# Kernel optimization log

Measured on AMD Instinct MI355X. Metric: run time of the kernel, lower is better.

## Reference

```python
import jax, jax.numpy as jnp
import numpy as np

N, E = 50000, 800000
NODE_DIM, EDGE_DIM, HIDDEN = 128, 32, 128


def setup_inputs() -> dict:
    key = jax.random.key(0)
    ks = jax.random.split(key, 12)
    def lin(k, fan_in, shape):
        bound = 1.0 / np.sqrt(fan_in)
        return jax.random.uniform(k, shape, jnp.float32, -bound, bound)
    return {
        "x": jax.random.normal(ks[0], (N, NODE_DIM), jnp.float32),
        "edge_index": jax.random.randint(ks[1], (2, E), 0, N),
        "edge_attr": jax.random.normal(ks[2], (E, EDGE_DIM), jnp.float32),
        # msg MLP: Linear(node+edge -> hidden), Linear(hidden -> hidden)
        "W1": lin(ks[3], NODE_DIM + EDGE_DIM, (HIDDEN, NODE_DIM + EDGE_DIM)),
        "b1": lin(ks[4], NODE_DIM + EDGE_DIM, (HIDDEN,)),
        "W2": lin(ks[5], HIDDEN, (HIDDEN, HIDDEN)),
        "b2": lin(ks[6], HIDDEN, (HIDDEN,)),
        # GRUCell(input=HIDDEN, hidden=NODE_DIM); gate order r,z,n (torch)
        "W_ih": lin(ks[7], NODE_DIM, (3 * NODE_DIM, HIDDEN)),
        "b_ih": lin(ks[8], NODE_DIM, (3 * NODE_DIM,)),
        "W_hh": lin(ks[9], NODE_DIM, (3 * NODE_DIM, NODE_DIM)),
        "b_hh": lin(ks[10], NODE_DIM, (3 * NODE_DIM,)),
    }


def reference(x, edge_index, edge_attr, W1, b1, W2, b2, W_ih, b_ih, W_hh, b_hh):
    src, dst = edge_index[0], edge_index[1]
    # gather + edge MLP: [E, node+edge] -> [E, hidden]
    m_in = jnp.concatenate([x[src], edge_attr], axis=-1)
    h1 = jax.nn.silu(m_in @ W1.T + b1)
    m = jax.nn.silu(h1 @ W2.T + b2)
    # scatter-add messages per destination node
    agg = jax.ops.segment_sum(m, dst, num_segments=x.shape[0])  # [N, hidden]
    # GRUCell: gates in torch order (r, z, n)
    gi = agg @ W_ih.T + b_ih  # [N, 3*node_dim]
    gh = x @ W_hh.T + b_hh
    i_r, i_z, i_n = jnp.split(gi, 3, axis=-1)
    h_r, h_z, h_n = jnp.split(gh, 3, axis=-1)
    r = jax.nn.sigmoid(i_r + h_r)
    z = jax.nn.sigmoid(i_z + h_z)
    n = jnp.tanh(i_n + r * h_n)
    return (1.0 - z) * n + z * x
```

## Files before the change

### kernel.cpp

```cpp
#include <hip/hip_runtime.h>
#include <hip/hip_bf16.h>
#include <cstdint>

typedef __bf16 bf16x8 __attribute__((ext_vector_type(8)));
typedef __bf16 bf16x4 __attribute__((ext_vector_type(4)));
typedef float  f32x4  __attribute__((ext_vector_type(4)));

#define ND 128
#define HID 128

__device__ __forceinline__ f32x4 mfma_bf16(bf16x8 a, bf16x8 b, f32x4 c) {
  return __builtin_amdgcn_mfma_f32_16x16x32_bf16(a, b, c, 0, 0, 0);
}
__device__ __forceinline__ float fast_sigmoid(float x) {
  return __fdividef(1.f, 1.f + __expf(-x));
}
__device__ __forceinline__ float fast_silu(float x) {
  return __fdividef(x, 1.f + __expf(-x));
}
__device__ __forceinline__ float fast_tanh(float x) {
  float cx = fminf(fmaxf(x, -15.f), 15.f);
  float e = __expf(2.f * cx);
  return __fdividef(e - 1.f, e + 1.f);
}

__global__ void cvt_all(const float* __restrict__ s0, __bf16* __restrict__ d0, int c1,
                        const float* __restrict__ s1, __bf16* __restrict__ d1, int c2,
                        const float* __restrict__ s2, __bf16* __restrict__ d2, int c3,
                        const float* __restrict__ s3, __bf16* __restrict__ d3, int c4,
                        const float* __restrict__ s4, __bf16* __restrict__ d4, int c5) {
  int i = blockIdx.x * blockDim.x + threadIdx.x;
  const float* s; __bf16* d; int j;
  if (i < c1)      { s = s0; d = d0; j = i; }
  else if (i < c2) { s = s1; d = d1; j = i - c1; }
  else if (i < c3) { s = s2; d = d2; j = i - c2; }
  else if (i < c4) { s = s3; d = d3; j = i - c3; }
  else if (i < c5) { s = s4; d = d4; j = i - c4; }
  else return;
  const float4* sp = reinterpret_cast<const float4*>(s) + (size_t)j * 2;
  float4 a = sp[0], b = sp[1];
  bf16x8 v;
  v[0] = (__bf16)a.x; v[1] = (__bf16)a.y; v[2] = (__bf16)a.z; v[3] = (__bf16)a.w;
  v[4] = (__bf16)b.x; v[5] = (__bf16)b.y; v[6] = (__bf16)b.z; v[7] = (__bf16)b.w;
  reinterpret_cast<bf16x8*>(d)[j] = v;
}

__global__ void k_hist(const int* __restrict__ dst, int* __restrict__ counts, int E) {
  int e = blockIdx.x * 256 + threadIdx.x;
  if (e < E) atomicAdd(&counts[dst[e]], 1);
}

__global__ void k_blocksum(const int* __restrict__ counts, int* __restrict__ bsum) {
  __shared__ int sd[256];
  int t = threadIdx.x;
  sd[t] = counts[blockIdx.x * 256 + t];
  __syncthreads();
  for (int d = 128; d > 0; d >>= 1) { if (t < d) sd[t] += sd[t + d]; __syncthreads(); }
  if (!t) bsum[blockIdx.x] = sd[0];
}

__global__ void k_scan_bsum(int* __restrict__ bsum, int nb) {
  __shared__ int sd[256];
  int t = threadIdx.x;
  int v = (t < nb) ? bsum[t] : 0;
  sd[t] = v;
  __syncthreads();
  for (int d = 1; d < 256; d <<= 1) {
    int u = (t >= d) ? sd[t - d] : 0;
    __syncthreads();
    sd[t] += u;
    __syncthreads();
  }
  if (t < nb) bsum[t] = sd[t] - v;
}

__global__ void k_scan_write(const int* __restrict__ counts, const int* __restrict__ bsum,
                             int* __restrict__ cursor) {
  __shared__ int sd[256];
  int t = threadIdx.x, b = blockIdx.x;
  int i = b * 256 + t;
  int c = counts[i];
  sd[t] = c;
  __syncthreads();
  for (int d = 1; d < 256; d <<= 1) {
    int u = (t >= d) ? sd[t - d] : 0;
    __syncthreads();
    sd[t] += u;
    __syncthreads();
  }
  cursor[i] = bsum[b] + sd[t] - c;
}

__global__ void k_perm(const int* __restrict__ dst, int* __restrict__ cursor,
                       int* __restrict__ eperm, int* __restrict__ dsorted, int E) {
  int e = blockIdx.x * 256 + threadIdx.x;
  if (e < E) {
    int d = dst[e];
    int p = atomicAdd(&cursor[d], 1);
    eperm[p] = e;
    dsorted[p] = d;
  }
}

#define TILE_E 64

__global__ __launch_bounds__(512, 4) void edge_mlp2(
    const __bf16* __restrict__ xb,
    const int*    __restrict__ srcp,
    const float*  __restrict__ ea,
    const __bf16* __restrict__ W1b,
    const float*  __restrict__ b1,
    const __bf16* __restrict__ W2b,
    const float*  __restrict__ b2,
    const int*    __restrict__ eperm,
    const int*    __restrict__ dsorted,
    float* __restrict__ agg,
    int ntiles)
{
  __shared__ __bf16 Als[TILE_E * 160];
  __shared__ __bf16 H1[TILE_E * 128];
  __shared__ int dstls[TILE_E];
  char* AB = (char*)Als;
  char* HB = (char*)H1;

  const int tid = threadIdx.x;
  const int w  = tid >> 6;
  const int l  = tid & 63;
  const int l4 = l >> 4;
  const int lm = l & 15;
  const int jb = w * 16;

  bf16x8 bw1[5], bw2[4];
  {
    const int jr = jb + lm;
#pragma unroll
    for (int kt = 0; kt < 5; ++kt)
      bw1[kt] = *reinterpret_cast<const bf16x8*>(W1b + (size_t)jr * 160 + kt * 32 + l4 * 8);
#pragma unroll
    for (int kt = 0; kt < 4; ++kt)
      bw2[kt] = *reinterpret_cast<const bf16x8*>(W2b + (size_t)jr * 128 + kt * 32 + l4 * 8);
  }
  const float4 b1v = *reinterpret_cast<const float4*>(b1 + jb + l4 * 4);
  const float4 b2v = *reinterpret_cast<const float4*>(b2 + jb + l4 * 4);

  const int fj = tid & 127;
  const int fg = tid >> 7;
  const int fchunk = fj >> 3;
  const int finner = (fj & 7) * 2;

  const int xslot = tid >> 4, xq = tid & 15;
  const int aslot = tid >> 3, aq = tid & 7;

  bf16x8 pxv0 = {}, pxv1 = {};
  float4 pea_ = {};
  int pdst_ = 0;

  auto PREFETCH = [&](int t) {
    int p0 = t * TILE_E;
    int e0i = eperm[p0 + xslot];
    int e1i = eperm[p0 + xslot + 32];
    int s0 = srcp[e0i];
    int s1 = srcp[e1i];
    pxv0 = *reinterpret_cast<const bf16x8*>(xb + (size_t)s0 * ND + xq * 8);
    pxv1 = *reinterpret_cast<const bf16x8*>(xb + (size_t)s1 * ND + xq * 8);
    int e2i = eperm[p0 + aslot];
    pea_ = reinterpret_cast<const float4*>(ea)[(size_t)e2i * 8 + aq];
    if (tid < TILE_E) pdst_ = dsorted[p0 + tid];
  };

  int tile = blockIdx.x;
  if (tile < ntiles) PREFETCH(tile);

  for (; tile < ntiles; tile += gridDim.x) {
    __syncthreads();

    {
      int s_ = xslot;
      *reinterpret_cast<bf16x8*>(AB + s_ * 320 + ((xq ^ (s_ & 7)) << 4)) = pxv0;
      int s2 = xslot + 32;
      *reinterpret_cast<bf16x8*>(AB + s2 * 320 + ((xq ^ (s2 & 7)) << 4)) = pxv1;
    }
    {
      bf16x4 h;
      h[0] = (__bf16)pea_.x; h[1] = (__bf16)pea_.y;
      h[2] = (__bf16)pea_.z; h[3] = (__bf16)pea_.w;
      int pc = 16 + ((aq >> 1) ^ (aslot & 3));
      *reinterpret_cast<bf16x4*>(AB + aslot * 320 + (pc << 4) + ((aq & 1) << 3)) = h;
    }
    if (tid < TILE_E) dstls[tid] = pdst_;
    __syncthreads();

    int nt = tile + gridDim.x;
    if (nt < ntiles) PREFETCH(nt);

#pragma unroll
    for (int et = 0; et < 4; ++et) {
      const int s_ = et * 16 + lm;
      const int sw = s_ & 7;
      f32x4 acc = {0.f, 0.f, 0.f, 0.f};
#pragma unroll
      for (int kt = 0; kt < 4; ++kt) {
        bf16x8 bfrag = *reinterpret_cast<const bf16x8*>(AB + s_ * 320 + (((kt * 4 + l4) ^ sw) << 4));
        acc = mfma_bf16(bw1[kt], bfrag, acc);
      }
      {
        bf16x8 bfrag = *reinterpret_cast<const bf16x8*>(AB + s_ * 320 + ((16 + (l4 ^ (s_ & 3))) << 4));
        acc = mfma_bf16(bw1[4], bfrag, acc);
      }
      bf16x4 h0;
#pragma unroll
      for (int rr = 0; rr < 4; ++rr)
        h0[rr] = (__bf16)fast_silu(acc[rr] + (&b1v.x)[rr]);
      int c0 = w * 2 + (l4 >> 1);
      int inner = (l4 & 1) << 3;
      *reinterpret_cast<bf16x4*>(HB + s_ * 256 + ((c0 ^ sw) << 4) + inner) = h0;
    }
    __syncthreads();

#pragma unroll
    for (int et = 0; et < 4; ++et) {
      const int s_ = et * 16 + lm;
      const int sw = s_ & 7;
      f32x4 acc = {0.f, 0.f, 0.f, 0.f};
#pragma unroll
      for (int kt = 0; kt < 4; ++kt) {
        bf16x8 bfrag = *reinterpret_cast<const bf16x8*>(HB + s_ * 256 + (((kt * 4 + l4) ^ sw) << 4));
        acc = mfma_bf16(bw2[kt], bfrag, acc);
      }
      bf16x4 m0;
#pragma unroll
      for (int rr = 0; rr < 4; ++rr)
        m0[rr] = (__bf16)fast_silu(acc[rr] + (&b2v.x)[rr]);
      int c0 = w * 2 + (l4 >> 1);
      int inner = (l4 & 1) << 3;
      *reinterpret_cast<bf16x4*>(AB + s_ * 256 + ((c0 ^ sw) << 4) + inner) = m0;
    }
    __syncthreads();

    {
      float acc = 0.f;
      int cur = dstls[fg * 16];
#pragma unroll
      for (int i = 0; i < 16; ++i) {
        int slot = fg * 16 + i;
        int nd = dstls[slot];
        if (nd != cur) {
          atomicAdd(agg + (size_t)cur * HID + fj, acc);
          acc = 0.f;
          cur = nd;
        }
        uint32_t raw = *reinterpret_cast<const uint16_t*>(
            AB + slot * 256 + ((fchunk ^ (slot & 7)) << 4) + finner);
        acc += __uint_as_float(raw << 16);
      }
      atomicAdd(agg + (size_t)cur * HID + fj, acc);
    }
  }
}

__global__ __launch_bounds__(512) void gru2(
    const float*  __restrict__ agg,
    const __bf16* __restrict__ xb,
    const float*  __restrict__ x,
    const __bf16* __restrict__ Wih, const float* __restrict__ bih,
    const __bf16* __restrict__ Whh, const float* __restrict__ bhh,
    float* __restrict__ out, int N)
{
  const int tid = threadIdx.x;
  const int w = tid >> 6, l = tid & 63;
  const int l4 = l >> 4, lm = l & 15;
  const int n0 = blockIdx.x * 64;
  const int jb = w * 16;
  const int jr = jb + lm, jz = jr + 128, jn = jr + 256;

  bf16x8 WiR[4], WhR[4], WiZ[4], WhZ[4], WiN[4], WhN[4];
#pragma unroll
  for (int kt = 0; kt < 4; ++kt) {
    int ko = kt * 32 + l4 * 8;
    WiR[kt] = *reinterpret_cast<const bf16x8*>(Wih + (size_t)jr * ND + ko);
    WhR[kt] = *reinterpret_cast<const bf16x8*>(Whh + (size_t)jr * ND + ko);
    WiZ[kt] = *reinterpret_cast<const bf16x8*>(Wih + (size_t)jz * ND + ko);
    WhZ[kt] = *reinterpret_cast<const bf16x8*>(Whh + (size_t)jz * ND + ko);
    WiN[kt] = *reinterpret_cast<const bf16x8*>(Wih + (size_t)jn * ND + ko);
    WhN[kt] = *reinterpret_cast<const bf16x8*>(Whh + (size_t)jn * ND + ko);
  }
  float4 birv, bizv, binv, bhnv;
  {
    int j0 = jb + l4 * 4;
    float4 a = *reinterpret_cast<const float4*>(bih + j0);
    float4 b = *reinterpret_cast<const float4*>(bhh + j0);
    birv = make_float4(a.x + b.x, a.y + b.y, a.z + b.z, a.w + b.w);
    a = *reinterpret_cast<const float4*>(bih + 128 + j0);
    b = *reinterpret_cast<const float4*>(bhh + 128 + j0);
    bizv = make_float4(a.x + b.x, a.y + b.y, a.z + b.z, a.w + b.w);
    binv = *reinterpret_cast<const float4*>(bih + 256 + j0);
    bhnv = *reinterpret_cast<const float4*>(bhh + 256 + j0);
  }

#pragma unroll
  for (int rt = 0; rt < 4; ++rt) {
    const int node = n0 + rt * 16 + lm;
    const bool ok = node < N;
    bf16x8 aA[4], aX[4];
#pragma unroll
    for (int kt = 0; kt < 4; ++kt) {
      int ko = kt * 32 + l4 * 8;
      bf16x8 z8 = {};
      if (ok) {
        float4 a0 = *reinterpret_cast<const float4*>(agg + (size_t)node * ND + ko);
        float4 a1 = *reinterpret_cast<const float4*>(agg + (size_t)node * ND + ko + 4);
        bf16x8 v;
        v[0] = (__bf16)a0.x; v[1] = (__bf16)a0.y; v[2] = (__bf16)a0.z; v[3] = (__bf16)a0.w;
        v[4] = (__bf16)a1.x; v[5] = (__bf16)a1.y; v[6] = (__bf16)a1.z; v[7] = (__bf16)a1.w;
        aA[kt] = v;
        aX[kt] = *reinterpret_cast<const bf16x8*>(xb + (size_t)node * ND + ko);
      } else {
        aA[kt] = z8;
        aX[kt] = z8;
      }
    }
    f32x4 aR = {0.f,0.f,0.f,0.f}, aZ = {0.f,0.f,0.f,0.f};
    f32x4 ai = {0.f,0.f,0.f,0.f}, ah = {0.f,0.f,0.f,0.f};
#pragma unroll
    for (int kt = 0; kt < 4; ++kt) {
      aR = mfma_bf16(WiR[kt], aA[kt], aR);
      aR = mfma_bf16(WhR[kt], aX[kt], aR);
      aZ = mfma_bf16(WiZ[kt], aA[kt], aZ);
      aZ = mfma_bf16(WhZ[kt], aX[kt], aZ);
      ai = mfma_bf16(WiN[kt], aA[kt], ai);
      ah = mfma_bf16(WhN[kt], aX[kt], ah);
    }
    if (ok) {
      float4 xv = *reinterpret_cast<const float4*>(x + (size_t)node * ND + jb + l4 * 4);
      float4 ov;
#pragma unroll
      for (int rr = 0; rr < 4; ++rr) {
        float r = fast_sigmoid(aR[rr] + (&birv.x)[rr]);
        float z = fast_sigmoid(aZ[rr] + (&bizv.x)[rr]);
        float n = fast_tanh(ai[rr] + (&binv.x)[rr] + r * (ah[rr] + (&bhnv.x)[rr]));
        (&ov.x)[rr] = (1.f - z) * n + z * (&xv.x)[rr];
      }
      *reinterpret_cast<float4*>(out + (size_t)node * ND + jb + l4 * 4) = ov;
    }
  }
}

extern "C" void kernel_launch(void* const* d_in, const int* in_sizes, int n_in,
                              void* d_out, int out_size, void* d_ws, size_t ws_size,
                              hipStream_t stream) {
  const float* x   = (const float*)d_in[0];
  const int*   ei  = (const int*)d_in[1];
  const float* ea  = (const float*)d_in[2];
  const float* W1  = (const float*)d_in[3];
  const float* b1  = (const float*)d_in[4];
  const float* W2  = (const float*)d_in[5];
  const float* b2  = (const float*)d_in[6];
  const float* Wih = (const float*)d_in[7];
  const float* bih = (const float*)d_in[8];
  const float* Whh = (const float*)d_in[9];
  const float* bhh = (const float*)d_in[10];
  float* out = (float*)d_out;
  const int N = in_sizes[0] / ND;
  const int E = in_sizes[1] / 2;

  const int nb = (N + 255) / 256;
  const int nC = nb * 256;

  char* ws = (char*)d_ws;
  size_t off = 0;
  auto alloc = [&](size_t bytes) -> void* {
    void* p = ws + off;
    off += (bytes + 255) & ~(size_t)255;
    return p;
  };
  __bf16* xb      = (__bf16*)alloc((size_t)N * ND * 2);
  __bf16* W1b     = (__bf16*)alloc(128 * 160 * 2);
  __bf16* W2b     = (__bf16*)alloc(128 * 128 * 2);
  __bf16* Wihb    = (__bf16*)alloc(384 * 128 * 2);
  __bf16* Whhb    = (__bf16*)alloc(384 * 128 * 2);
  int*    counts  = (int*)alloc((size_t)nC * 4);
  int*    cursor  = (int*)alloc((size_t)nC * 4);
  int*    bsum    = (int*)alloc(256 * 4);
  int*    eperm   = (int*)alloc((size_t)E * 4);
  int*    dsorted = (int*)alloc((size_t)E * 4);
  float*  agg     = (float*)alloc((size_t)N * ND * 4);
  (void)ws_size;

  const int* srcp = ei;
  const int* dstp = ei + E;

  hipMemsetAsync(agg, 0, (size_t)N * ND * 4, stream);
  hipMemsetAsync(counts, 0, (size_t)nC * 4, stream);

  const int n8_x = N * ND / 8, n8_1 = 128 * 160 / 8, n8_2 = 128 * 128 / 8, n8_g = 384 * 128 / 8;
  int c1 = n8_x, c2 = c1 + n8_1, c3 = c2 + n8_2, c4 = c3 + n8_g, c5 = c4 + n8_g;
  cvt_all<<<(c5 + 255) / 256, 256, 0, stream>>>(x, xb, c1, W1, W1b, c2, W2, W2b, c3,
                                                Wih, Wihb, c4, Whh, Whhb, c5);

  k_hist<<<(E + 255) / 256, 256, 0, stream>>>(dstp, counts, E);
  k_blocksum<<<nb, 256, 0, stream>>>(counts, bsum);
  k_scan_bsum<<<1, 256, 0, stream>>>(bsum, nb);
  k_scan_write<<<nb, 256, 0, stream>>>(counts, bsum, cursor);
  k_perm<<<(E + 255) / 256, 256, 0, stream>>>(dstp, cursor, eperm, dsorted, E);

  const int ntiles = E / TILE_E;
  edge_mlp2<<<2500, 512, 0, stream>>>(xb, srcp, ea, W1b, b1, W2b, b2,
                                      eperm, dsorted, agg, ntiles);

  gru2<<<(N + 63) / 64, 512, 0, stream>>>(agg, xb, x, Wihb, bih, Whhb, bhh, out, N);
}
```

Before: 365.8 us.

## Switch edge MLP to 32x32x16 MFMA tiles and restructure scatter reduction

The edge MLP kernel now uses 32x32x16 bf16 MFMA, with each wave computing a 32-hidden by 32-edge tile instead of four 16x16 tiles. Bias is preloaded into the accumulator, and the LDS swizzle widens to 16 chunks. The segmented scatter-add now runs on only four waves, each lane holding two columns and reading dst via readlane. Edge-attribute loads are deferred, so only the index is prefetched. Together these aim to cut MFMA issue count and LDS reads per edge, at the cost of more weight registers, which may hurt occupancy. Bias is also rounded to bf16, which slightly lowers precision.

```diff
diff --git a/kernel.cpp b/kernel.cpp
--- a/kernel.cpp
+++ b/kernel.cpp
@@ -5,12 +5,14 @@
 typedef __bf16 bf16x8 __attribute__((ext_vector_type(8)));
 typedef __bf16 bf16x4 __attribute__((ext_vector_type(4)));
 typedef float  f32x4  __attribute__((ext_vector_type(4)));
+typedef float  f32x16 __attribute__((ext_vector_type(16)));
+typedef unsigned short u16x16 __attribute__((ext_vector_type(16)));
 
 #define ND 128
 #define HID 128
 
-__device__ __forceinline__ f32x4 mfma_bf16(bf16x8 a, bf16x8 b, f32x4 c) {
-  return __builtin_amdgcn_mfma_f32_16x16x32_bf16(a, b, c, 0, 0, 0);
+__device__ __forceinline__ f32x16 mfma32(bf16x8 a, bf16x8 b, f32x16 c) {
+  return __builtin_amdgcn_mfma_f32_32x32x16_bf16(a, b, c, 0, 0, 0);
 }
 __device__ __forceinline__ float fast_sigmoid(float x) {
   return __fdividef(1.f, 1.f + __expf(-x));
@@ -22,6 +24,9 @@
   float cx = fminf(fmaxf(x, -15.f), 15.f);
   float e = __expf(2.f * cx);
   return __fdividef(e - 1.f, e + 1.f);
+}
+__device__ __forceinline__ f32x4 mfma_bf16(bf16x8 a, bf16x8 b, f32x4 c) {
+  return __builtin_amdgcn_mfma_f32_16x16x32_bf16(a, b, c, 0, 0, 0);
 }
 
 __global__ void cvt_all(const float* __restrict__ s0, __bf16* __restrict__ d0, int c1,
@@ -104,7 +109,7 @@
 
 #define TILE_E 64
 
-__global__ __launch_bounds__(512, 4) void edge_mlp2(
+__global__ __launch_bounds__(512, 4) void edge_mlp3(
     const __bf16* __restrict__ xb,
     const int*    __restrict__ srcp,
     const float*  __restrict__ ea,
@@ -124,47 +129,49 @@
   char* HB = (char*)H1;
 
   const int tid = threadIdx.x;
-  const int w  = tid >> 6;
-  const int l  = tid & 63;
-  const int l4 = l >> 4;
-  const int lm = l & 15;
-  const int jb = w * 16;
-
-  bf16x8 bw1[5], bw2[4];
+  const int w   = tid >> 6;
+  const int l   = tid & 63;
+  const int hi  = l >> 5;
+  const int sl  = l & 31;
+  const int jb  = (w & 3) * 32;
+  const int sh  = (w >> 2) * 32;
+  const int s   = sh + sl;
+  const int sw  = s & 15;
+
+  bf16x8 bw1[10], bw2[8];
   {
-    const int jr = jb + lm;
-#pragma unroll
-    for (int kt = 0; kt < 5; ++kt)
-      bw1[kt] = *reinterpret_cast<const bf16x8*>(W1b + (size_t)jr * 160 + kt * 32 + l4 * 8);
-#pragma unroll
-    for (int kt = 0; kt < 4; ++kt)
-      bw2[kt] = *reinterpret_cast<const bf16x8*>(W2b + (size_t)jr * 128 + kt * 32 + l4 * 8);
-  }
-  const float4 b1v = *reinterpret_cast<const float4*>(b1 + jb + l4 * 4);
-  const float4 b2v = *reinterpret_cast<const float4*>(b2 + jb + l4 * 4);
-
-  const int fj = tid & 127;
-  const int fg = tid >> 7;
-  const int fchunk = fj >> 3;
-  const int finner = (fj & 7) * 2;
+    const int jr = jb + sl;
+#pragma unroll
+    for (int kt = 0; kt < 10; ++kt)
+      bw1[kt] = *reinterpret_cast<const bf16x8*>(W1b + (size_t)jr * 160 + kt * 16 + hi * 8);
+#pragma unroll
+    for (int kt = 0; kt < 8; ++kt)
+      bw2[kt] = *reinterpret_cast<const bf16x8*>(W2b + (size_t)jr * 128 + kt * 16 + hi * 8);
+  }
+  u16x16 b1p, b2p;
+#pragma unroll
+  for (int g = 0; g < 4; ++g) {
+#pragma unroll
+    for (int r = 0; r < 4; ++r) {
+      int j = jb + g * 8 + 4 * hi + r;
+      b1p[g * 4 + r] = (unsigned short)(__builtin_bit_cast(unsigned int, b1[j]) >> 16);
+      b2p[g * 4 + r] = (unsigned short)(__builtin_bit_cast(unsigned int, b2[j]) >> 16);
+    }
+  }
 
   const int xslot = tid >> 4, xq = tid & 15;
   const int aslot = tid >> 3, aq = tid & 7;
 
   bf16x8 pxv0 = {}, pxv1 = {};
-  float4 pea_ = {};
-  int pdst_ = 0;
+  int peaidx = 0, pdst_ = 0;
 
   auto PREFETCH = [&](int t) {
     int p0 = t * TILE_E;
-    int e0i = eperm[p0 + xslot];
-    int e1i = eperm[p0 + xslot + 32];
-    int s0 = srcp[e0i];
-    int s1 = srcp[e1i];
+    int s0 = srcp[eperm[p0 + xslot]];
+    int s1 = srcp[eperm[p0 + xslot + 32]];
     pxv0 = *reinterpret_cast<const bf16x8*>(xb + (size_t)s0 * ND + xq * 8);
     pxv1 = *reinterpret_cast<const bf16x8*>(xb + (size_t)s1 * ND + xq * 8);
-    int e2i = eperm[p0 + aslot];
-    pea_ = reinterpret_cast<const float4*>(ea)[(size_t)e2i * 8 + aq];
+    peaidx = eperm[p0 + aslot];
     if (tid < TILE_E) pdst_ = dsorted[p0 + tid];
   };
 
@@ -175,15 +182,14 @@
     __syncthreads();
 
     {
-      int s_ = xslot;
-      *reinterpret_cast<bf16x8*>(AB + s_ * 320 + ((xq ^ (s_ & 7)) << 4)) = pxv0;
-      int s2 = xslot + 32;
-      *reinterpret_cast<bf16x8*>(AB + s2 * 320 + ((xq ^ (s2 & 7)) << 4)) = pxv1;
+      *reinterpret_cast<bf16x8*>(AB + xslot * 320 + ((xq ^ (xslot & 15)) << 4)) = pxv0;
+      int x2 = xslot + 32;
+      *reinterpret_cast<bf16x8*>(AB + x2 * 320 + ((xq ^ (x2 & 15)) << 4)) = pxv1;
     }
     {
+      float4 v = reinterpret_cast<const float4*>(ea)[(size_t)peaidx * 8 + aq];
       bf16x4 h;
-      h[0] = (__bf16)pea_.x; h[1] = (__bf16)pea_.y;
-      h[2] = (__bf16)pea_.z; h[3] = (__bf16)pea_.w;
+      h[0] = (__bf16)v.x; h[1] = (__bf16)v.y; h[2] = (__bf16)v.z; h[3] = (__bf16)v.w;
       int pc = 16 + ((aq >> 1) ^ (aslot & 3));
       *reinterpret_cast<bf16x4*>(AB + aslot * 320 + (pc << 4) + ((aq & 1) << 3)) = h;
     }
@@ -193,67 +199,72 @@
     int nt = tile + gridDim.x;
     if (nt < ntiles) PREFETCH(nt);
 
-#pragma unroll
-    for (int et = 0; et < 4; ++et) {
-      const int s_ = et * 16 + lm;
-      const int sw = s_ & 7;
-      f32x4 acc = {0.f, 0.f, 0.f, 0.f};
-#pragma unroll
-      for (int kt = 0; kt < 4; ++kt) {
-        bf16x8 bfrag = *reinterpret_cast<const bf16x8*>(AB + s_ * 320 + (((kt * 4 + l4) ^ sw) << 4));
-        acc = mfma_bf16(bw1[kt], bfrag, acc);
-      }
-      {
-        bf16x8 bfrag = *reinterpret_cast<const bf16x8*>(AB + s_ * 320 + ((16 + (l4 ^ (s_ & 3))) << 4));
-        acc = mfma_bf16(bw1[4], bfrag, acc);
-      }
-      bf16x4 h0;
-#pragma unroll
-      for (int rr = 0; rr < 4; ++rr)
-        h0[rr] = (__bf16)fast_silu(acc[rr] + (&b1v.x)[rr]);
-      int c0 = w * 2 + (l4 >> 1);
-      int inner = (l4 & 1) << 3;
-      *reinterpret_cast<bf16x4*>(HB + s_ * 256 + ((c0 ^ sw) << 4) + inner) = h0;
-    }
-    __syncthreads();
-
-#pragma unroll
-    for (int et = 0; et < 4; ++et) {
-      const int s_ = et * 16 + lm;
-      const int sw = s_ & 7;
-      f32x4 acc = {0.f, 0.f, 0.f, 0.f};
-#pragma unroll
-      for (int kt = 0; kt < 4; ++kt) {
-        bf16x8 bfrag = *reinterpret_cast<const bf16x8*>(HB + s_ * 256 + (((kt * 4 + l4) ^ sw) << 4));
-        acc = mfma_bf16(bw2[kt], bfrag, acc);
-      }
-      bf16x4 m0;
-#pragma unroll
-      for (int rr = 0; rr < 4; ++rr)
-        m0[rr] = (__bf16)fast_silu(acc[rr] + (&b2v.x)[rr]);
-      int c0 = w * 2 + (l4 >> 1);
-      int inner = (l4 & 1) << 3;
-      *reinterpret_cast<bf16x4*>(AB + s_ * 256 + ((c0 ^ sw) << 4) + inner) = m0;
-    }
-    __syncthreads();
-
     {
-      float acc = 0.f;
-      int cur = dstls[fg * 16];
+      f32x16 acc;
+#pragma unroll
+      for (int i = 0; i < 16; ++i)
+        acc[i] = __uint_as_float(((unsigned int)b1p[i]) << 16);
+#pragma unroll
+      for (int kt = 0; kt < 8; ++kt) {
+        bf16x8 bf = *reinterpret_cast<const bf16x8*>(AB + s * 320 + (((2 * kt + hi) ^ sw) << 4));
+        acc = mfma32(bw1[kt], bf, acc);
+      }
+#pragma unroll
+      for (int kt = 0; kt < 2; ++kt) {
+        bf16x8 bf = *reinterpret_cast<const bf16x8*>(AB + s * 320 + ((16 + ((2 * kt + hi) ^ (s & 3))) << 4));
+        acc = mfma32(bw1[8 + kt], bf, acc);
+      }
+#pragma unroll
+      for (int g = 0; g < 4; ++g) {
+        bf16x4 h;
+#pragma unroll
+        for (int r = 0; r < 4; ++r) h[r] = (__bf16)fast_silu(acc[4 * g + r]);
+        *reinterpret_cast<bf16x4*>(HB + s * 256 + ((((jb >> 3) + g) ^ sw) << 4) + 8 * hi) = h;
+      }
+    }
+    __syncthreads();
+
+    {
+      f32x16 acc;
+#pragma unroll
+      for (int i = 0; i < 16; ++i)
+        acc[i] = __uint_as_float(((unsigned int)b2p[i]) << 16);
+#pragma unroll
+      for (int kt = 0; kt < 8; ++kt) {
+        bf16x8 bf = *reinterpret_cast<const bf16x8*>(HB + s * 256 + (((2 * kt + hi) ^ sw) << 4));
+        acc = mfma32(bw2[kt], bf, acc);
+      }
+#pragma unroll
+      for (int g = 0; g < 4; ++g) {
+        bf16x4 m;
+#pragma unroll
+        for (int r = 0; r < 4; ++r) m[r] = (__bf16)fast_silu(acc[4 * g + r]);
+        *reinterpret_cast<bf16x4*>(AB + s * 256 + ((((jb >> 3) + g) ^ sw) << 4) + 8 * hi) = m;
+      }
+    }
+    __syncthreads();
+
+    if (w < 4) {
+      const int base = w * 16;
+      int myd = dstls[base + (l & 15)];
+      float a0 = 0.f, a1 = 0.f;
+      int cur = __builtin_amdgcn_readlane(myd, 0);
 #pragma unroll
       for (int i = 0; i < 16; ++i) {
-        int slot = fg * 16 + i;
-        int nd = dstls[slot];
+        int nd = __builtin_amdgcn_readlane(myd, i);
         if (nd != cur) {
-          atomicAdd(agg + (size_t)cur * HID + fj, acc);
-          acc = 0.f;
-          cur = nd;
+          atomicAdd(agg + (size_t)cur * HID + l * 2, a0);
+          atomicAdd(agg + (size_t)cur * HID + l * 2 + 1, a1);
+          a0 = 0.f; a1 = 0.f; cur = nd;
         }
-        uint32_t raw = *reinterpret_cast<const uint16_t*>(
-            AB + slot * 256 + ((fchunk ^ (slot & 7)) << 4) + finner);
-        acc += __uint_as_float(raw << 16);
-      }
-      atomicAdd(agg + (size_t)cur * HID + fj, acc);
+        int ss = base + i;
+        uint32_t u = *reinterpret_cast<const uint32_t*>(
+            AB + ss * 256 + ((((l >> 2)) ^ (ss & 15)) << 4) + ((l & 3) << 2));
+        a0 += __uint_as_float(u << 16);
+        a1 += __uint_as_float(u & 0xffff0000u);
+      }
+      atomicAdd(agg + (size_t)cur * HID + l * 2, a0);
+      atomicAdd(agg + (size_t)cur * HID + l * 2 + 1, a1);
     }
   }
 }
@@ -404,7 +415,7 @@
   k_perm<<<(E + 255) / 256, 256, 0, stream>>>(dstp, cursor, eperm, dsorted, E);
 
   const int ntiles = E / TILE_E;
-  edge_mlp2<<<2500, 512, 0, stream>>>(xb, srcp, ea, W1b, b1, W2b, b2,
+  edge_mlp3<<<2500, 512, 0, stream>>>(xb, srcp, ea, W1b, b1, W2b, b2,
                                       eperm, dsorted, agg, ntiles);
 
   gru2<<<(N + 63) / 64, 512, 0, stream>>>(agg, xb, x, Wihb, bih, Whhb, bhh, out, N);
```

Result: slower. 614.8 us (+68.1%).

## Rework edge scatter to wave-per-segment pairs and make GRU kernel persistent

Applied to the files above, without the earlier changes.

The scatter-add stage of the edge kernel now uses only four waves, each handling 16 sorted slots. Every lane reads two packed bf16 values per slot with one 32-bit LDS load, and destination ids are broadcast with readlane instead of per-thread LDS loads. The GRU kernel becomes a grid-stride loop over 256 blocks, so its per-block weight register loads are amortized over many node tiles. The edge kernel's launch bounds drop from 4 to 2 blocks per CU, which allows more registers per thread but may lower occupancy; half the waves now sit idle during the scatter.

```diff
diff --git a/kernel.cpp b/kernel.cpp
--- a/kernel.cpp
+++ b/kernel.cpp
@@ -104,7 +104,7 @@
 
 #define TILE_E 64
 
-__global__ __launch_bounds__(512, 4) void edge_mlp2(
+__global__ __launch_bounds__(512, 2) void edge_mlp6(
     const __bf16* __restrict__ xb,
     const int*    __restrict__ srcp,
     const float*  __restrict__ ea,
@@ -143,11 +143,6 @@
   const float4 b1v = *reinterpret_cast<const float4*>(b1 + jb + l4 * 4);
   const float4 b2v = *reinterpret_cast<const float4*>(b2 + jb + l4 * 4);
 
-  const int fj = tid & 127;
-  const int fg = tid >> 7;
-  const int fchunk = fj >> 3;
-  const int finner = (fj & 7) * 2;
-
   const int xslot = tid >> 4, xq = tid & 15;
   const int aslot = tid >> 3, aq = tid & 7;
 
@@ -237,39 +232,42 @@
     }
     __syncthreads();
 
-    {
-      float acc = 0.f;
-      int cur = dstls[fg * 16];
+    if (w < 4) {
+      const int base = w * 16;
+      int myd = dstls[base + (l & 15)];
+      float a0 = 0.f, a1 = 0.f;
+      int cur = __builtin_amdgcn_readlane(myd, 0);
 #pragma unroll
       for (int i = 0; i < 16; ++i) {
-        int slot = fg * 16 + i;
-        int nd = dstls[slot];
+        int nd = __builtin_amdgcn_readlane(myd, i);
         if (nd != cur) {
-          atomicAdd(agg + (size_t)cur * HID + fj, acc);
-          acc = 0.f;
-          cur = nd;
+          atomicAdd(agg + (size_t)cur * HID + l * 2, a0);
+          atomicAdd(agg + (size_t)cur * HID + l * 2 + 1, a1);
+          a0 = 0.f; a1 = 0.f; cur = nd;
         }
-        uint32_t raw = *reinterpret_cast<const uint16_t*>(
-            AB + slot * 256 + ((fchunk ^ (slot & 7)) << 4) + finner);
-        acc += __uint_as_float(raw << 16);
-      }
-      atomicAdd(agg + (size_t)cur * HID + fj, acc);
-    }
-  }
-}
-
-__global__ __launch_bounds__(512) void gru2(
+        int ss = base + i;
+        uint32_t u = *reinterpret_cast<const uint32_t*>(
+            AB + ss * 256 + (((l >> 2) ^ (ss & 7)) << 4) + ((l & 3) << 2));
+        a0 += __uint_as_float(u << 16);
+        a1 += __uint_as_float(u & 0xffff0000u);
+      }
+      atomicAdd(agg + (size_t)cur * HID + l * 2, a0);
+      atomicAdd(agg + (size_t)cur * HID + l * 2 + 1, a1);
+    }
+  }
+}
+
+__global__ __launch_bounds__(512) void gru3(
     const float*  __restrict__ agg,
     const __bf16* __restrict__ xb,
     const float*  __restrict__ x,
     const __bf16* __restrict__ Wih, const float* __restrict__ bih,
     const __bf16* __restrict__ Whh, const float* __restrict__ bhh,
-    float* __restrict__ out, int N)
+    float* __restrict__ out, int N, int ntilesN)
 {
   const int tid = threadIdx.x;
   const int w = tid >> 6, l = tid & 63;
   const int l4 = l >> 4, lm = l & 15;
-  const int n0 = blockIdx.x * 64;
   const int jb = w * 16;
   const int jr = jb + lm, jz = jr + 128, jn = jr + 256;
 
@@ -297,50 +295,53 @@
     bhnv = *reinterpret_cast<const float4*>(bhh + 256 + j0);
   }
 
-#pragma unroll
-  for (int rt = 0; rt < 4; ++rt) {
-    const int node = n0 + rt * 16 + lm;
-    const bool ok = node < N;
-    bf16x8 aA[4], aX[4];
-#pragma unroll
-    for (int kt = 0; kt < 4; ++kt) {
-      int ko = kt * 32 + l4 * 8;
-      bf16x8 z8 = {};
+  for (int bt = blockIdx.x; bt < ntilesN; bt += gridDim.x) {
+    const int n0 = bt * 64;
+#pragma unroll
+    for (int rt = 0; rt < 4; ++rt) {
+      const int node = n0 + rt * 16 + lm;
+      const bool ok = node < N;
+      bf16x8 aA[4], aX[4];
+#pragma unroll
+      for (int kt = 0; kt < 4; ++kt) {
+        int ko = kt * 32 + l4 * 8;
+        bf16x8 z8 = {};
+        if (ok) {
+          float4 a0 = *reinterpret_cast<const float4*>(agg + (size_t)node * ND + ko);
+          float4 a1 = *reinterpret_cast<const float4*>(agg + (size_t)node * ND + ko + 4);
+          bf16x8 v;
+          v[0] = (__bf16)a0.x; v[1] = (__bf16)a0.y; v[2] = (__bf16)a0.z; v[3] = (__bf16)a0.w;
+          v[4] = (__bf16)a1.x; v[5] = (__bf16)a1.y; v[6] = (__bf16)a1.z; v[7] = (__bf16)a1.w;
+          aA[kt] = v;
+          aX[kt] = *reinterpret_cast<const bf16x8*>(xb + (size_t)node * ND + ko);
+        } else {
+          aA[kt] = z8;
+          aX[kt] = z8;
+        }
+      }
+      f32x4 aR = {0.f,0.f,0.f,0.f}, aZ = {0.f,0.f,0.f,0.f};
+      f32x4 ai = {0.f,0.f,0.f,0.f}, ah = {0.f,0.f,0.f,0.f};
+#pragma unroll
+      for (int kt = 0; kt < 4; ++kt) {
+        aR = mfma_bf16(WiR[kt], aA[kt], aR);
+        aR = mfma_bf16(WhR[kt], aX[kt], aR);
+        aZ = mfma_bf16(WiZ[kt], aA[kt], aZ);
+        aZ = mfma_bf16(WhZ[kt], aX[kt], aZ);
+        ai = mfma_bf16(WiN[kt], aA[kt], ai);
+        ah = mfma_bf16(WhN[kt], aX[kt], ah);
+      }
       if (ok) {
-        float4 a0 = *reinterpret_cast<const float4*>(agg + (size_t)node * ND + ko);
-        float4 a1 = *reinterpret_cast<const float4*>(agg + (size_t)node * ND + ko + 4);
-        bf16x8 v;
-        v[0] = (__bf16)a0.x; v[1] = (__bf16)a0.y; v[2] = (__bf16)a0.z; v[3] = (__bf16)a0.w;
-        v[4] = (__bf16)a1.x; v[5] = (__bf16)a1.y; v[6] = (__bf16)a1.z; v[7] = (__bf16)a1.w;
-        aA[kt] = v;
-        aX[kt] = *reinterpret_cast<const bf16x8*>(xb + (size_t)node * ND + ko);
-      } else {
-        aA[kt] = z8;
-        aX[kt] = z8;
-      }
-    }
-    f32x4 aR = {0.f,0.f,0.f,0.f}, aZ = {0.f,0.f,0.f,0.f};
-    f32x4 ai = {0.f,0.f,0.f,0.f}, ah = {0.f,0.f,0.f,0.f};
-#pragma unroll
-    for (int kt = 0; kt < 4; ++kt) {
-      aR = mfma_bf16(WiR[kt], aA[kt], aR);
-      aR = mfma_bf16(WhR[kt], aX[kt], aR);
-      aZ = mfma_bf16(WiZ[kt], aA[kt], aZ);
-      aZ = mfma_bf16(WhZ[kt], aX[kt], aZ);
-      ai = mfma_bf16(WiN[kt], aA[kt], ai);
-      ah = mfma_bf16(WhN[kt], aX[kt], ah);
-    }
-    if (ok) {
-      float4 xv = *reinterpret_cast<const float4*>(x + (size_t)node * ND + jb + l4 * 4);
-      float4 ov;
-#pragma unroll
-      for (int rr = 0; rr < 4; ++rr) {
-        float r = fast_sigmoid(aR[rr] + (&birv.x)[rr]);
-        float z = fast_sigmoid(aZ[rr] + (&bizv.x)[rr]);
-        float n = fast_tanh(ai[rr] + (&binv.x)[rr] + r * (ah[rr] + (&bhnv.x)[rr]));
-        (&ov.x)[rr] = (1.f - z) * n + z * (&xv.x)[rr];
-      }
-      *reinterpret_cast<float4*>(out + (size_t)node * ND + jb + l4 * 4) = ov;
+        float4 xv = *reinterpret_cast<const float4*>(x + (size_t)node * ND + jb + l4 * 4);
+        float4 ov;
+#pragma unroll
+        for (int rr = 0; rr < 4; ++rr) {
+          float r = fast_sigmoid(aR[rr] + (&birv.x)[rr]);
+          float z = fast_sigmoid(aZ[rr] + (&bizv.x)[rr]);
+          float n = fast_tanh(ai[rr] + (&binv.x)[rr] + r * (ah[rr] + (&bhnv.x)[rr]));
+          (&ov.x)[rr] = (1.f - z) * n + z * (&xv.x)[rr];
+        }
+        *reinterpret_cast<float4*>(out + (size_t)node * ND + jb + l4 * 4) = ov;
+      }
     }
   }
 }
@@ -404,8 +405,9 @@
   k_perm<<<(E + 255) / 256, 256, 0, stream>>>(dstp, cursor, eperm, dsorted, E);
 
   const int ntiles = E / TILE_E;
-  edge_mlp2<<<2500, 512, 0, stream>>>(xb, srcp, ea, W1b, b1, W2b, b2,
+  edge_mlp6<<<2500, 512, 0, stream>>>(xb, srcp, ea, W1b, b1, W2b, b2,
                                       eperm, dsorted, agg, ntiles);
 
-  gru2<<<(N + 63) / 64, 512, 0, stream>>>(agg, xb, x, Wihb, bih, Whhb, bhh, out, N);
-}
+  const int ntilesN = (N + 63) / 64;
+  gru3<<<256, 512, 0, stream>>>(agg, xb, x, Wihb, bih, Whhb, bhh, out, N, ntilesN);
+}
```

After: 413.2 us. 1.13x slower.
